# Optimization experiments

Hardware: AMD Instinct MI355X
Metric: run time of the kernel (lower is better)

Reference implementation:

```python
import jax, jax.numpy as jnp
import numpy as np

K = 1024
H = 128

def setup_inputs() -> dict:
    key = jax.random.key(0)
    ks = jax.random.split(key, 11)
    s = lambda fan_in: 1.0 / np.sqrt(fan_in)
    # coord_mlp: Linear(H, H//2) -> GELU -> Linear(H//2, 2)
    cW1 = jax.random.uniform(ks[0], (H, H // 2), minval=-s(H), maxval=s(H))
    cb1 = jax.random.uniform(ks[1], (H // 2,), minval=-s(H), maxval=s(H))
    cW2 = jax.random.uniform(ks[2], (H // 2, 2), minval=-s(H // 2), maxval=s(H // 2))
    cb2 = jax.random.uniform(ks[3], (2,), minval=-s(H // 2), maxval=s(H // 2))
    # edge_mlp: Linear(2H, H) -> GELU -> Linear(H, H//2) -> GELU -> Linear(H//2, 1)
    eW1 = jax.random.uniform(ks[4], (2 * H, H), minval=-s(2 * H), maxval=s(2 * H))
    eb1 = jax.random.uniform(ks[5], (H,), minval=-s(2 * H), maxval=s(2 * H))
    eW2 = jax.random.uniform(ks[6], (H, H // 2), minval=-s(H), maxval=s(H))
    eb2 = jax.random.uniform(ks[7], (H // 2,), minval=-s(H), maxval=s(H))
    eW3 = jax.random.uniform(ks[8], (H // 2, 1), minval=-s(H // 2), maxval=s(H // 2))
    eb3 = jax.random.uniform(ks[9], (1,), minval=-s(H // 2), maxval=s(H // 2))
    z_s = jax.random.normal(ks[10], (K, H), dtype=jnp.float32)
    return {"z_s": z_s, "cW1": cW1, "cb1": cb1, "cW2": cW2, "cb2": cb2,
            "eW1": eW1, "eb1": eb1, "eW2": eW2, "eb2": eb2, "eW3": eW3, "eb3": eb3}

def reference(z_s, cW1, cb1, cW2, cb2, eW1, eb1, eW2, eb2, eW3, eb3):
    gelu = lambda x: jax.nn.gelu(x, approximate=False)  # torch default GELU is exact erf form
    # coords: [k, 2]
    coords_pred = gelu(z_s @ cW1 + cb1) @ cW2 + cb2
    # edge first layer: cat([zi, zj]) @ eW1 == zi @ eW1[:H] + zj @ eW1[H:]
    # (same math as the broadcast-concat, without materializing [k, k, 2H])
    pi = z_s @ eW1[:H]   # [k, H]
    pj = z_s @ eW1[H:]   # [k, H]
    h1 = gelu(pi[:, None, :] + pj[None, :, :] + eb1)   # [k, k, H]
    h2 = gelu(h1 @ eW2 + eb2)                          # [k, k, H//2]
    adj_logits = (h2 @ eW3 + eb3)[..., 0]              # [k, k]
    adj_logits = (adj_logits + adj_logits.T) / 2.0
    return (coords_pred, adj_logits)
```

## Files before the change

kernel.cpp:

```cpp
#include <hip/hip_runtime.h>
#include <hip/hip_fp16.h>


#define KN 1024
#define HN 128

typedef float  floatx4 __attribute__((ext_vector_type(4)));
typedef _Float16 half8v __attribute__((ext_vector_type(8)));

__device__ __forceinline__ float gelu_f(float x) {
    float x2 = x * x;
    float t  = fmaf(x2, -0.1029434f, -2.3022087f);
    float e  = __builtin_amdgcn_exp2f(x * t);
    return x * __builtin_amdgcn_rcpf(e + 1.0f);
}

__device__ __forceinline__ unsigned int gelu2u(unsigned int xu) {
    __half2 x  = __builtin_bit_cast(__half2, xu);
    __half2 x2 = __hmul2(x, x);
    __half2 t  = __hfma2(x2, __float2half2_rn(-0.1029434f),
                             __float2half2_rn(-2.3022087f));
    __half2 e  = h2exp2(__hmul2(x, t));
    __half2 r  = h2rcp(__hadd2(e, __float2half2_rn(1.0f)));
    return __builtin_bit_cast(unsigned int, __hmul2(x, r));
}

__global__ __launch_bounds__(256) void prep_kernel(
    const float* __restrict__ z,   const float* __restrict__ cW1,
    const float* __restrict__ cb1, const float* __restrict__ cW2,
    const float* __restrict__ cb2, const float* __restrict__ eW1,
    const float* __restrict__ eb1, const float* __restrict__ eW2,
    _Float16* __restrict__ pi_h,   _Float16* __restrict__ pj_h,
    _Float16* __restrict__ w2T,    float* __restrict__ coords ) {
    __shared__ float z8[8][128];
    __shared__ float c1s[8][64];
    const int tid = threadIdx.x;
    const int r0  = blockIdx.x * 8;

    if (blockIdx.x < 32) {
        int e = blockIdx.x * 256 + tid;
        w2T[e] = (_Float16)eW2[(e & 127) * 64 + (e >> 7)];
    }

#pragma unroll
    for (int s = 0; s < 4; ++s) {
        int e = tid + 256 * s;
        z8[e >> 7][e & 127] = z[r0 * HN + e];
    }
    __syncthreads();

    const int col = tid & 127, which = tid >> 7;
    const float* w = eW1 + which * HN * HN + col;
    float acc8[8] = {0.f, 0.f, 0.f, 0.f, 0.f, 0.f, 0.f, 0.f};
    for (int k = 0; k < HN; ++k) {
        float wv = w[k * HN];
#pragma unroll
        for (int r = 0; r < 8; ++r) acc8[r] = fmaf(z8[r][k], wv, acc8[r]);
    }
    if (which == 0) {
        float b = eb1[col];
#pragma unroll
        for (int r = 0; r < 8; ++r)
            pi_h[(r0 + r) * HN + col] = (_Float16)(acc8[r] + b);
    } else {
#pragma unroll
        for (int r = 0; r < 8; ++r)
            pj_h[(r0 + r) * HN + col] = (_Float16)acc8[r];
    }

#pragma unroll
    for (int s = 0; s < 2; ++s) {
        int task = tid + 256 * s;
        int row = task >> 6, mid = task & 63;
        float a = cb1[mid];
        for (int k = 0; k < HN; ++k) a = fmaf(z8[row][k], cW1[k * 64 + mid], a);
        c1s[row][mid] = gelu_f(a);
    }
    __syncthreads();
    if (tid < 16) {
        int row = tid >> 1, o = tid & 1;
        float a = cb2[o];
#pragma unroll 8
        for (int m = 0; m < 64; ++m) a = fmaf(c1s[row][m], cW2[m * 2 + o], a);
        coords[(r0 + row) * 2 + o] = a;
    }
}

__global__ __launch_bounds__(512, 7) void edge_kernel(
    const _Float16* __restrict__ pi_h, const _Float16* __restrict__ pj_h,
    const _Float16* __restrict__ w2T,  const float* __restrict__ eb2,
    const float* __restrict__ eW3,     const float* __restrict__ eb3,
    float* __restrict__ out_adj) {
    __shared__ __align__(16) unsigned int pi_s[32 * 64];
    __shared__ __align__(16) unsigned int pj_s[16 * 64];
    __shared__ __align__(16) unsigned int w2_s[64 * 64];
    const int i0 = blockIdx.y * 32, j0 = blockIdx.x * 16;
    const int tid = threadIdx.x;

    const unsigned int* piu = (const unsigned int*)pi_h;
    const unsigned int* pju = (const unsigned int*)pj_h;
    const unsigned int* w2u = (const unsigned int*)w2T;

#pragma unroll
    for (int s = 0; s < 4; ++s) {
        int e = tid + 512 * s;
        int r = e >> 6;
        pi_s[e ^ ((r & 7) << 2)] = piu[(i0 + r) * 64 + (e & 63)];
    }
#pragma unroll
    for (int s = 0; s < 2; ++s) {
        int e = tid + 512 * s;
        int r = e >> 6;
        pj_s[e ^ ((r & 7) << 2)] = pju[(j0 + r) * 64 + (e & 63)];
    }
#pragma unroll
    for (int s = 0; s < 8; ++s) {
        int e = tid + 512 * s;
        int r = e >> 6;
        w2_s[e ^ ((r & 7) << 2)] = w2u[e];
    }

    const int lane = tid & 63;
    const int wave = tid >> 6;
    const int lrow = lane & 15;
    const int lhi  = lane >> 4;
    const int lhi4 = lhi << 2;
    const int swzJ = (lrow & 7) << 2;

    const unsigned int* pjrow  = &pj_s[lrow << 6];
    const unsigned int* w2base = &w2_s[lrow << 6];

    float eb2_l[4], w3_l[4];
#pragma unroll
    for (int c = 0; c < 4; ++c) {
        eb2_l[c] = eb2[c * 16 + lrow];
        w3_l[c]  = eW3[c * 16 + lrow];
    }
    const float b3 = eb3[0];
    __syncthreads();

#pragma unroll
    for (int t = 0; t < 4; ++t) {
        const int iL = (wave << 2) + t;
        const unsigned int* pirow = &pi_s[iL << 6];
        const int swzI = (iL & 7) << 2;

        floatx4 acc[4];
#pragma unroll
        for (int c = 0; c < 4; ++c) acc[c] = (floatx4){0.f, 0.f, 0.f, 0.f};

#pragma unroll
        for (int q = 0; q < 4; ++q) {
            const int ko = (q << 4) + lhi4;
            half8v a = *reinterpret_cast<const half8v*>(&pirow[ko ^ swzI]);
            half8v b = *reinterpret_cast<const half8v*>(&pjrow[ko ^ swzJ]);
            uint4 su = __builtin_bit_cast(uint4, a + b);
            uint4 gu;
            gu.x = gelu2u(su.x);
            gu.y = gelu2u(su.y);
            gu.z = gelu2u(su.z);
            gu.w = gelu2u(su.w);
            half8v af = __builtin_bit_cast(half8v, gu);
            const int kw = ko ^ swzJ;
#pragma unroll
            for (int c = 0; c < 4; ++c) {
                half8v bf = *reinterpret_cast<const half8v*>(
                    &w2base[(c << 10) + kw]);
                acc[c] = __builtin_amdgcn_mfma_f32_16x16x32_f16(
                    af, bf, acc[c], 0, 0, 0);
            }
        }

        float tv[4];
#pragma unroll
        for (int m = 0; m < 4; ++m) {
            float s = 0.f;
#pragma unroll
            for (int c = 0; c < 4; ++c)
                s = fmaf(gelu_f(acc[c][m] + eb2_l[c]), w3_l[c], s);
            s += __shfl_xor(s, 1);
            s += __shfl_xor(s, 2);
            s += __shfl_xor(s, 4);
            s += __shfl_xor(s, 8);
            tv[m] = s + b3;
        }
        if (lrow == 0) {
            float4 v = make_float4(tv[0], tv[1], tv[2], tv[3]);
            *reinterpret_cast<float4*>(
                &out_adj[(size_t)(i0 + iL) * KN + j0 + lhi4]) = v;
        }
    }
}

__global__ __launch_bounds__(256) void sym_kernel(float* __restrict__ adj) {
    int idx = blockIdx.x * 256 + threadIdx.x;
    int i = idx >> 10, j = idx & 1023;
    if (j < i) return;
    float a = adj[i * KN + j];
    float b = adj[j * KN + i];
    float m = 0.5f * (a + b);
    adj[i * KN + j] = m;
    adj[j * KN + i] = m;
}

extern "C" void kernel_launch(void* const* d_in, const int* in_sizes, int n_in,
                              void* d_out, int out_size, void* d_ws, size_t ws_size,
                              hipStream_t stream) {
    const float* z   = (const float*)d_in[0];
    const float* cW1 = (const float*)d_in[1];
    const float* cb1 = (const float*)d_in[2];
    const float* cW2 = (const float*)d_in[3];
    const float* cb2 = (const float*)d_in[4];
    const float* eW1 = (const float*)d_in[5];
    const float* eb1 = (const float*)d_in[6];
    const float* eW2 = (const float*)d_in[7];
    const float* eb2 = (const float*)d_in[8];
    const float* eW3 = (const float*)d_in[9];
    const float* eb3 = (const float*)d_in[10];

    float* out = (float*)d_out;
    _Float16* pi_h = (_Float16*)d_ws;
    _Float16* pj_h = pi_h + KN * HN;
    _Float16* w2T  = pj_h + KN * HN;

    prep_kernel<<<128, 256, 0, stream>>>(z, cW1, cb1, cW2, cb2, eW1, eb1, eW2,
                                         pi_h, pj_h, w2T, out);

    dim3 gridB(64, 32);
    edge_kernel<<<gridB, 512, 0, stream>>>(pi_h, pj_h, w2T, eb2, eW3, eb3,
                                           out + 2048);

    sym_kernel<<<4096, 256, 0, stream>>>(out + 2048);
}
```

Measured before the change: 82.85 us.

## Compute final edge layer with MFMA and fp16 packed GELU on transposed accumulators

Swaps the MFMA operand order so accumulators hold hidden units along the register dimension, and permutes the rows of the W2 weight matrix in the prep kernel to match. The bias is folded into the accumulator init. The second GELU now runs in packed fp16 and the H/2→1 projection becomes two MFMAs against an fp16 copy of W3. This replaces the per-element fp32 GELU and the cross-lane shuffle reduction, at the cost of extra fp16 rounding in the second layer's activations.

```diff
diff --git a/kernel.cpp b/kernel.cpp
--- a/kernel.cpp
+++ b/kernel.cpp
@@ -7,6 +7,7 @@
 
 typedef float  floatx4 __attribute__((ext_vector_type(4)));
 typedef _Float16 half8v __attribute__((ext_vector_type(8)));
+typedef _Float16 half2v __attribute__((ext_vector_type(2)));
 
 __device__ __forceinline__ float gelu_f(float x) {
     float x2 = x * x;
@@ -25,13 +26,19 @@
     return __builtin_bit_cast(unsigned int, __hmul2(x, r));
 }
 
+__device__ __forceinline__ unsigned int cvt2u(float a, float b) {
+    return __builtin_bit_cast(unsigned int, __builtin_amdgcn_cvt_pkrtz(a, b));
+}
+
 __global__ __launch_bounds__(256) void prep_kernel(
     const float* __restrict__ z,   const float* __restrict__ cW1,
     const float* __restrict__ cb1, const float* __restrict__ cW2,
     const float* __restrict__ cb2, const float* __restrict__ eW1,
     const float* __restrict__ eb1, const float* __restrict__ eW2,
+    const float* __restrict__ eW3,
     _Float16* __restrict__ pi_h,   _Float16* __restrict__ pj_h,
-    _Float16* __restrict__ w2T,    float* __restrict__ coords ) {
+    _Float16* __restrict__ w2T,    _Float16* __restrict__ w3h,
+    float* __restrict__ coords ) {
     __shared__ float z8[8][128];
     __shared__ float c1s[8][64];
     const int tid = threadIdx.x;
@@ -39,8 +46,12 @@
 
     if (blockIdx.x < 32) {
         int e = blockIdx.x * 256 + tid;
-        w2T[e] = (_Float16)eW2[(e & 127) * 64 + (e >> 7)];
-    }
+        int d = e >> 7, k = e & 127;
+        int R = ((d >> 5) & 1) * 32 + ((d >> 2) & 1) * 16 +
+                ((d >> 3) & 3) * 4  + (d & 3);
+        w2T[R * 128 + k] = (_Float16)eW2[k * 64 + d];
+    }
+    if (blockIdx.x == 32 && tid < 64) w3h[tid] = (_Float16)eW3[tid];
 
 #pragma unroll
     for (int s = 0; s < 4; ++s) {
@@ -88,8 +99,8 @@
 
 __global__ __launch_bounds__(512, 7) void edge_kernel(
     const _Float16* __restrict__ pi_h, const _Float16* __restrict__ pj_h,
-    const _Float16* __restrict__ w2T,  const float* __restrict__ eb2,
-    const float* __restrict__ eW3,     const float* __restrict__ eb3,
+    const _Float16* __restrict__ w2T,  const _Float16* __restrict__ w3h,
+    const float* __restrict__ eb2,     const float* __restrict__ eb3,
     float* __restrict__ out_adj) {
     __shared__ __align__(16) unsigned int pi_s[32 * 64];
     __shared__ __align__(16) unsigned int pj_s[16 * 64];
@@ -125,17 +136,18 @@
     const int lrow = lane & 15;
     const int lhi  = lane >> 4;
     const int lhi4 = lhi << 2;
+    const int lhi8 = lhi << 3;
     const int swzJ = (lrow & 7) << 2;
 
     const unsigned int* pjrow  = &pj_s[lrow << 6];
     const unsigned int* w2base = &w2_s[lrow << 6];
 
-    float eb2_l[4], w3_l[4];
-#pragma unroll
-    for (int c = 0; c < 4; ++c) {
-        eb2_l[c] = eb2[c * 16 + lrow];
-        w3_l[c]  = eW3[c * 16 + lrow];
-    }
+    const half8v w3f0 = *reinterpret_cast<const half8v*>(&w3h[lhi8]);
+    const half8v w3f1 = *reinterpret_cast<const half8v*>(&w3h[32 + lhi8]);
+    const float4 e0 = *reinterpret_cast<const float4*>(&eb2[lhi8]);
+    const float4 e1 = *reinterpret_cast<const float4*>(&eb2[lhi8 + 4]);
+    const float4 e2 = *reinterpret_cast<const float4*>(&eb2[32 + lhi8]);
+    const float4 e3 = *reinterpret_cast<const float4*>(&eb2[36 + lhi8]);
     const float b3 = eb3[0];
     __syncthreads();
 
@@ -146,8 +158,10 @@
         const int swzI = (iL & 7) << 2;
 
         floatx4 acc[4];
-#pragma unroll
-        for (int c = 0; c < 4; ++c) acc[c] = (floatx4){0.f, 0.f, 0.f, 0.f};
+        acc[0] = (floatx4){e0.x, e0.y, e0.z, e0.w};
+        acc[1] = (floatx4){e1.x, e1.y, e1.z, e1.w};
+        acc[2] = (floatx4){e2.x, e2.y, e2.z, e2.w};
+        acc[3] = (floatx4){e3.x, e3.y, e3.z, e3.w};
 
 #pragma unroll
         for (int q = 0; q < 4; ++q) {
@@ -167,28 +181,27 @@
                 half8v bf = *reinterpret_cast<const half8v*>(
                     &w2base[(c << 10) + kw]);
                 acc[c] = __builtin_amdgcn_mfma_f32_16x16x32_f16(
-                    af, bf, acc[c], 0, 0, 0);
+                    bf, af, acc[c], 0, 0, 0);
             }
         }
 
-        float tv[4];
-#pragma unroll
-        for (int m = 0; m < 4; ++m) {
-            float s = 0.f;
-#pragma unroll
-            for (int c = 0; c < 4; ++c)
-                s = fmaf(gelu_f(acc[c][m] + eb2_l[c]), w3_l[c], s);
-            s += __shfl_xor(s, 1);
-            s += __shfl_xor(s, 2);
-            s += __shfl_xor(s, 4);
-            s += __shfl_xor(s, 8);
-            tv[m] = s + b3;
-        }
-        if (lrow == 0) {
-            float4 v = make_float4(tv[0], tv[1], tv[2], tv[3]);
-            *reinterpret_cast<float4*>(
-                &out_adj[(size_t)(i0 + iL) * KN + j0 + lhi4]) = v;
-        }
+        uint4 u0, u1;
+        u0.x = gelu2u(cvt2u(acc[0][0], acc[0][1]));
+        u0.y = gelu2u(cvt2u(acc[0][2], acc[0][3]));
+        u0.z = gelu2u(cvt2u(acc[1][0], acc[1][1]));
+        u0.w = gelu2u(cvt2u(acc[1][2], acc[1][3]));
+        u1.x = gelu2u(cvt2u(acc[2][0], acc[2][1]));
+        u1.y = gelu2u(cvt2u(acc[2][2], acc[2][3]));
+        u1.z = gelu2u(cvt2u(acc[3][0], acc[3][1]));
+        u1.w = gelu2u(cvt2u(acc[3][2], acc[3][3]));
+        half8v h20 = __builtin_bit_cast(half8v, u0);
+        half8v h21 = __builtin_bit_cast(half8v, u1);
+
+        floatx4 d = (floatx4){b3, b3, b3, b3};
+        d = __builtin_amdgcn_mfma_f32_16x16x32_f16(w3f0, h20, d, 0, 0, 0);
+        d = __builtin_amdgcn_mfma_f32_16x16x32_f16(w3f1, h21, d, 0, 0, 0);
+        if (lhi == 0)
+            out_adj[(size_t)(i0 + iL) * KN + j0 + lrow] = d[0];
     }
 }
 
@@ -222,12 +235,13 @@
     _Float16* pi_h = (_Float16*)d_ws;
     _Float16* pj_h = pi_h + KN * HN;
     _Float16* w2T  = pj_h + KN * HN;
+    _Float16* w3h  = w2T + 64 * HN;
 
     prep_kernel<<<128, 256, 0, stream>>>(z, cW1, cb1, cW2, cb2, eW1, eb1, eW2,
-                                         pi_h, pj_h, w2T, out);
+                                         eW3, pi_h, pj_h, w2T, w3h, out);
 
     dim3 gridB(64, 32);
-    edge_kernel<<<gridB, 512, 0, stream>>>(pi_h, pj_h, w2T, eb2, eW3, eb3,
+    edge_kernel<<<gridB, 512, 0, stream>>>(pi_h, pj_h, w2T, w3h, eb2, eb3,
                                            out + 2048);
 
     sym_kernel<<<4096, 256, 0, stream>>>(out + 2048);
```

After: 79.48 us. -4.1%, faster.
